# Kernel optimization log

Measured on AMD Instinct MI355X. Metric: run time of the kernel, lower is better.

The kernel has to match this reference:

```python
import jax, jax.numpy as jnp
import numpy as np

D_MODEL = 1024
HEADS = 16


def setup_inputs() -> dict:
    key = jax.random.key(0)
    ks = jax.random.split(key, 5)
    S = 4096
    x = jax.random.normal(ks[0], (S, D_MODEL), dtype=jnp.float32)
    scale = 1.0 / np.sqrt(D_MODEL)
    Wq = jax.random.normal(ks[1], (D_MODEL, D_MODEL), dtype=jnp.float32) * scale
    Wk = jax.random.normal(ks[2], (D_MODEL, D_MODEL), dtype=jnp.float32) * scale
    Wv = jax.random.normal(ks[3], (D_MODEL, D_MODEL), dtype=jnp.float32) * scale
    Wo = jax.random.normal(ks[4], (D_MODEL, D_MODEL), dtype=jnp.float32) * scale
    return {"x": x, "Wq": Wq, "Wk": Wk, "Wv": Wv, "Wo": Wo}


def reference(x, Wq, Wk, Wv, Wo):
    # x: [S, D]; weights follow torch Linear convention y = x @ W.T
    S, D = x.shape
    H = HEADS
    d_k = D // H
    q = (x @ Wq.T).reshape(S, H, d_k)  # [S,H,dk]
    k = (x @ Wk.T).reshape(S, H, d_k)
    v = (x @ Wv.T).reshape(S, H, d_k)
    # logits: [H, S, S] = q k^T / sqrt(d_k)
    logits = jnp.einsum('shd,thd->hst', q, k) / jnp.sqrt(jnp.asarray(d_k, x.dtype))
    probs = jax.nn.softmax(logits, axis=-1)
    out = jnp.einsum('hst,thd->shd', probs, v).reshape(S, D)
    return out @ Wo.T
```

## Files before the change

### kernel.cpp

```cpp
#include <hip/hip_runtime.h>
#include <hip/hip_bf16.h>


typedef __bf16 bf16_t;
typedef __bf16 bf16x8 __attribute__((ext_vector_type(8)));
typedef __bf16 bf16x4 __attribute__((ext_vector_type(4)));
typedef float f32x4 __attribute__((ext_vector_type(4)));

#define D_MODEL 1024
#define SEQ 4096
#define HEADS 16
#define DK 64
#define QSCALE 0.1803368801111204f

__global__ void cast_kernel(const float* __restrict__ in, bf16_t* __restrict__ out, int n) {
    int i = (blockIdx.x * blockDim.x + threadIdx.x) * 4;
    if (i < n) {
        float4 v = *(const float4*)(in + i);
        bf16x4 o;
        o[0] = (bf16_t)v.x; o[1] = (bf16_t)v.y; o[2] = (bf16_t)v.z; o[3] = (bf16_t)v.w;
        *(bf16x4*)(out + i) = o;
    }
}

__global__ void cast4_kernel(const float* __restrict__ a, const float* __restrict__ b,
                             const float* __restrict__ c, const float* __restrict__ d,
                             bf16_t* __restrict__ out) {
    int gi = blockIdx.x * blockDim.x + threadIdx.x;
    int which = gi >> 18;
    int i = (gi & 0x3FFFF) * 4;
    const float* src = which == 0 ? a : which == 1 ? b : which == 2 ? c : d;
    float4 v = *(const float4*)(src + i);
    bf16x4 o;
    o[0] = (bf16_t)v.x; o[1] = (bf16_t)v.y; o[2] = (bf16_t)v.z; o[3] = (bf16_t)v.w;
    *(bf16x4*)(out + (size_t)which * D_MODEL * D_MODEL + i) = o;
}

__device__ __forceinline__ void g2l16(const bf16_t* g, bf16_t* l) {
    __builtin_amdgcn_global_load_lds(
        (const __attribute__((address_space(1))) void*)g,
        (__attribute__((address_space(3))) void*)l, 16, 0, 0);
}

__device__ __forceinline__ bf16x8 exp2_pk(const f32x4 a, const f32x4 b) {
    int v[8];
#pragma unroll
    for (int r = 0; r < 4; r++) {
        v[r]     = (int)fmaf(a[r], 128.0f, 16250.99f);
        v[r + 4] = (int)fmaf(b[r], 128.0f, 16250.99f);
    }
    union { int u[4]; bf16x8 h; } o;
#pragma unroll
    for (int p = 0; p < 4; p++) o.u[p] = v[2 * p] | (v[2 * p + 1] << 16);
    return o.h;
}

template <int ROUTE>
__global__ __launch_bounds__(256, 4) void gemm_lds(const bf16_t* __restrict__ A,
                                                   const bf16_t* __restrict__ B,
                                                   void* __restrict__ out0,
                                                   void* __restrict__ out1,
                                                   void* __restrict__ out2,
                                                   int M, int N, int K) {
    __shared__ __align__(16) bf16_t As[128 * 64];
    __shared__ __align__(16) bf16_t Bs[64 * 64];

    const int tid = threadIdx.x;
    const int lane = tid & 63;
    const int wave = tid >> 6;
    const int l15 = lane & 15;
    const int lg  = lane >> 4;
    const int m0 = blockIdx.y * 128;
    const int n0 = blockIdx.x * 64;
    const int wm = (wave >> 1) * 64;
    const int wn = (wave & 1) * 32;

    const bf16_t* aSrc[4]; bf16_t* aDst[4];
#pragma unroll
    for (int it = 0; it < 4; it++) {
        int c = it * 256 + tid;
        int row = c >> 3, cc = (c & 7) ^ (row & 7);
        aSrc[it] = A + (size_t)(m0 + row) * K + cc * 8;
        aDst[it] = As + c * 8;
    }
    const bf16_t* bSrc[2]; bf16_t* bDst[2];
#pragma unroll
    for (int it = 0; it < 2; it++) {
        int c = it * 256 + tid;
        int row = c >> 3, cc = (c & 7) ^ (row & 7);
        bSrc[it] = B + (size_t)(n0 + row) * K + cc * 8;
        bDst[it] = Bs + c * 8;
    }

    int aoff[2][4], boff[2][2];
#pragma unroll
    for (int kk = 0; kk < 2; kk++) {
#pragma unroll
        for (int i = 0; i < 4; i++) {
            int row = wm + i * 16 + l15;
            aoff[kk][i] = row * 64 + (((kk << 2) | lg) ^ (row & 7)) * 8;
        }
#pragma unroll
        for (int j = 0; j < 2; j++) {
            int row = wn + j * 16 + l15;
            boff[kk][j] = row * 64 + (((kk << 2) | lg) ^ (row & 7)) * 8;
        }
    }

    f32x4 acc[4][2];
#pragma unroll
    for (int i = 0; i < 4; i++)
#pragma unroll
        for (int j = 0; j < 2; j++) acc[i][j] = f32x4{0.f, 0.f, 0.f, 0.f};

    for (int k0 = 0; k0 < K; k0 += 64) {
#pragma unroll
        for (int it = 0; it < 4; it++) g2l16(aSrc[it] + k0, aDst[it]);
#pragma unroll
        for (int it = 0; it < 2; it++) g2l16(bSrc[it] + k0, bDst[it]);
        __syncthreads();

#pragma unroll
        for (int kk = 0; kk < 2; kk++) {
            bf16x8 af[4], bfm[2];
#pragma unroll
            for (int i = 0; i < 4; i++) af[i] = *(const bf16x8*)(As + aoff[kk][i]);
#pragma unroll
            for (int j = 0; j < 2; j++) bfm[j] = *(const bf16x8*)(Bs + boff[kk][j]);
#pragma unroll
            for (int i = 0; i < 4; i++)
#pragma unroll
                for (int j = 0; j < 2; j++)
                    acc[i][j] = __builtin_amdgcn_mfma_f32_16x16x32_bf16(af[i], bfm[j], acc[i][j], 0, 0, 0);
        }
        __syncthreads();
    }

    const int ng = n0 + wn;
    if (ROUTE == 0) {
        float* C = (float*)out0;
#pragma unroll
        for (int i = 0; i < 4; i++)
#pragma unroll
            for (int r = 0; r < 4; r++) {
                int m = m0 + wm + i * 16 + lg * 4 + r;
                float* crow = C + (size_t)m * N + ng;
#pragma unroll
                for (int j = 0; j < 2; j++) crow[j * 16 + l15] = acc[i][j][r];
            }
    } else {
        if (ng < 2048) {
            const bool isQ = (ng < 1024);
            const float sc = isQ ? QSCALE : 1.0f;
            bf16_t* dst = isQ ? (bf16_t*)out0 : (bf16_t*)out1;
            int nn = ng & 1023;
#pragma unroll
            for (int i = 0; i < 4; i++)
#pragma unroll
                for (int r = 0; r < 4; r++) {
                    int m = m0 + wm + i * 16 + lg * 4 + r;
                    bf16_t* crow = dst + (size_t)m * D_MODEL + nn;
#pragma unroll
                    for (int j = 0; j < 2; j++) crow[j * 16 + l15] = (bf16_t)(acc[i][j][r] * sc);
                }
        } else {
            bf16_t* Vt = (bf16_t*)out2;
#pragma unroll
            for (int i = 0; i < 4; i++)
#pragma unroll
                for (int j = 0; j < 2; j++) {
                    int vcol = ng - 2048 + j * 16 + l15;
                    int m = m0 + wm + i * 16 + lg * 4;
                    int mp = (m & ~31) | (((m >> 2) & 3) << 3) | (((m >> 4) & 1) << 2);
                    bf16x4 v4;
#pragma unroll
                    for (int r = 0; r < 4; r++) v4[r] = (bf16_t)acc[i][j][r];
                    *(bf16x4*)(Vt + (size_t)vcol * SEQ + mp) = v4;
                }
        }
    }
}

__global__ __launch_bounds__(256) void attn_kernel(const bf16_t* __restrict__ Q,
                                                   const bf16_t* __restrict__ Km,
                                                   const bf16_t* __restrict__ Vt,
                                                   bf16_t* __restrict__ O) {
    const int tid = threadIdx.x;
    const int lane = tid & 63;
    const int wave = tid >> 6;
    const int l15 = lane & 15;
    const int lg  = lane >> 4;
    const int bid = blockIdx.x;
    const int h    = (bid & 7) * 2 + ((bid >> 3) & 1);
    const int qblk = bid >> 4;
    const int q0 = qblk * 128;
    const int hoff = h * DK;

    __shared__ union {
        struct { __align__(16) bf16_t K[2][64 * 64]; __align__(16) bf16_t V[2][64 * 64]; } kv;
        __align__(16) bf16_t Ot[128][72];
    } sm;

    bf16x8 qf[2][2];
#pragma unroll
    for (int t = 0; t < 2; t++)
#pragma unroll
        for (int c = 0; c < 2; c++)
            qf[t][c] = *(const bf16x8*)(Q + (size_t)(q0 + wave * 32 + t * 16 + l15) * D_MODEL
                                        + hoff + c * 32 + lg * 8);

    f32x4 oacc[2][4], lfrag[2];
#pragma unroll
    for (int t = 0; t < 2; t++) {
        lfrag[t] = f32x4{0.f, 0.f, 0.f, 0.f};
#pragma unroll
        for (int dt = 0; dt < 4; dt++) oacc[t][dt] = f32x4{0.f, 0.f, 0.f, 0.f};
    }

    bf16x8 ones8;
#pragma unroll
    for (int j = 0; j < 8; j++) ones8[j] = (bf16_t)1.0f;

    const bf16_t* kSrc[2]; const bf16_t* vSrc[2];
#pragma unroll
    for (int it = 0; it < 2; it++) {
        int c = it * 256 + tid;
        int row = c >> 3, dc = (c & 7) ^ (row & 7);
        kSrc[it] = Km + (size_t)row * D_MODEL + hoff + dc * 8;
        vSrc[it] = Vt + (size_t)(hoff + row) * SEQ + dc * 8;
    }

    int kOff[4][2], vOff[2][4];
#pragma unroll
    for (int kt = 0; kt < 4; kt++)
#pragma unroll
        for (int c = 0; c < 2; c++) {
            int row = kt * 16 + l15;
            kOff[kt][c] = row * 64 + (((c * 4 + lg) ^ (row & 7)) * 8);
        }
#pragma unroll
    for (int kp = 0; kp < 2; kp++)
#pragma unroll
        for (int dt = 0; dt < 4; dt++) {
            int row = dt * 16 + l15;
            vOff[kp][dt] = row * 64 + (((kp * 4 + lg) ^ (row & 7)) * 8);
        }

#pragma unroll
    for (int it = 0; it < 2; it++) {
        g2l16(kSrc[it], &sm.kv.K[0][(it * 256 + tid) * 8]);
        g2l16(vSrc[it], &sm.kv.V[0][(it * 256 + tid) * 8]);
    }

    for (int s = 0; s < SEQ / 64; s++) {
        const int cur = s & 1;
        __syncthreads();

        if (s + 1 < SEQ / 64) {
            const int nxt = cur ^ 1;
#pragma unroll
            for (int it = 0; it < 2; it++) {
                g2l16(kSrc[it] + (size_t)(s + 1) * 64 * D_MODEL, &sm.kv.K[nxt][(it * 256 + tid) * 8]);
                g2l16(vSrc[it] + (s + 1) * 64,                   &sm.kv.V[nxt][(it * 256 + tid) * 8]);
            }
        }

        const bf16_t* Kb = sm.kv.K[cur];
        const bf16_t* Vb = sm.kv.V[cur];

#pragma unroll
        for (int kp = 0; kp < 2; kp++) {
            f32x4 st[2][2];
#pragma unroll
            for (int sub = 0; sub < 2; sub++) {
                const int kt = kp * 2 + sub;
                const bf16x8 kf0 = *(const bf16x8*)(Kb + kOff[kt][0]);
                const bf16x8 kf1 = *(const bf16x8*)(Kb + kOff[kt][1]);
#pragma unroll
                for (int t = 0; t < 2; t++) {
                    f32x4 a = f32x4{0.f, 0.f, 0.f, 0.f};
                    a = __builtin_amdgcn_mfma_f32_16x16x32_bf16(kf0, qf[t][0], a, 0, 0, 0);
                    a = __builtin_amdgcn_mfma_f32_16x16x32_bf16(kf1, qf[t][1], a, 0, 0, 0);
                    st[t][sub] = a;
                }
            }

            const bf16x8 pbig0 = exp2_pk(st[0][0], st[0][1]);
            const bf16x8 pbig1 = exp2_pk(st[1][0], st[1][1]);

            lfrag[0] = __builtin_amdgcn_mfma_f32_16x16x32_bf16(ones8, pbig0, lfrag[0], 0, 0, 0);
            lfrag[1] = __builtin_amdgcn_mfma_f32_16x16x32_bf16(ones8, pbig1, lfrag[1], 0, 0, 0);

#pragma unroll
            for (int dt = 0; dt < 4; dt++) {
                const bf16x8 vf = *(const bf16x8*)(Vb + vOff[kp][dt]);
                oacc[0][dt] = __builtin_amdgcn_mfma_f32_16x16x32_bf16(vf, pbig0, oacc[0][dt], 0, 0, 0);
                oacc[1][dt] = __builtin_amdgcn_mfma_f32_16x16x32_bf16(vf, pbig1, oacc[1][dt], 0, 0, 0);
            }
        }
    }
    __syncthreads();

#pragma unroll
    for (int t = 0; t < 2; t++) {
        float inv = 1.f / lfrag[t][0];
        const int qrow = wave * 32 + t * 16 + l15;
#pragma unroll
        for (int dt = 0; dt < 4; dt++)
#pragma unroll
            for (int r = 0; r < 4; r++)
                sm.Ot[qrow][dt * 16 + lg * 4 + r] = (bf16_t)(oacc[t][dt][r] * inv);
    }
    __syncthreads();

    {
        const int row = tid >> 1;
        const int half = tid & 1;
        bf16_t* orow = O + (size_t)(q0 + row) * D_MODEL + hoff + half * 32;
#pragma unroll
        for (int m = 0; m < 4; m++)
            *(bf16x8*)(orow + m * 8) = *(const bf16x8*)(&sm.Ot[row][half * 32 + m * 8]);
    }
}

extern "C" void kernel_launch(void* const* d_in, const int* in_sizes, int n_in,
                              void* d_out, int out_size, void* d_ws, size_t ws_size,
                              hipStream_t stream) {
    const float* x  = (const float*)d_in[0];
    const float* Wq = (const float*)d_in[1];
    const float* Wk = (const float*)d_in[2];
    const float* Wv = (const float*)d_in[3];
    const float* Wo = (const float*)d_in[4];
    float* out = (float*)d_out;

    char* ws = (char*)d_ws;
    bf16_t* xb  = (bf16_t*)(ws);
    bf16_t* wqb = (bf16_t*)(ws + (8u  << 20));
    bf16_t* wob = (bf16_t*)(ws + (14u << 20));
    bf16_t* Qb  = (bf16_t*)(ws + (16u << 20));
    bf16_t* Kb  = (bf16_t*)(ws + (24u << 20));
    bf16_t* Vtb = (bf16_t*)(ws + (32u << 20));
    bf16_t* Ab  = (bf16_t*)(ws + (40u << 20));

    const int nX = SEQ * D_MODEL;
    cast_kernel<<<nX / 4 / 256, 256, 0, stream>>>(x, xb, nX);
    cast4_kernel<<<4 * 1024, 256, 0, stream>>>(Wq, Wk, Wv, Wo, wqb);

    gemm_lds<1><<<dim3(3 * D_MODEL / 64, SEQ / 128), 256, 0, stream>>>(
        xb, wqb, Qb, Kb, Vtb, SEQ, 3 * D_MODEL, D_MODEL);

    attn_kernel<<<512, 256, 0, stream>>>(Qb, Kb, Vtb, Ab);

    gemm_lds<0><<<dim3(D_MODEL / 64, SEQ / 128), 256, 0, stream>>>(
        Ab, wob, out, nullptr, nullptr, SEQ, D_MODEL, D_MODEL);
}
```

Baseline: 213.0 us.

## Load attention K/V fragments directly from global into registers, drop LDS staging

The attention kernel no longer stages K and V tiles through LDS with barriers. Each wave now loads its MFMA fragments straight from global memory into registers, double-buffered across two register sets. The output epilogue also writes directly instead of transposing through shared memory, and the exp2 approximation is rewritten to use a float magic-add plus a byte-permute pack. This removes LDS traffic and __syncthreads, but every wave in a block now re-reads the same K/V from global/L2, and register pressure rises, which is why occupancy is lowered to 2.

```diff
diff --git a/kernel.cpp b/kernel.cpp
--- a/kernel.cpp
+++ b/kernel.cpp
@@ -12,6 +12,7 @@
 #define HEADS 16
 #define DK 64
 #define QSCALE 0.1803368801111204f
+#define EXP2_MAGIC 8404859.0f
 
 __global__ void cast_kernel(const float* __restrict__ in, bf16_t* __restrict__ out, int n) {
     int i = (blockIdx.x * blockDim.x + threadIdx.x) * 4;
@@ -43,15 +44,16 @@
 }
 
 __device__ __forceinline__ bf16x8 exp2_pk(const f32x4 a, const f32x4 b) {
-    int v[8];
+    union { float f; unsigned u; } v[8];
 #pragma unroll
     for (int r = 0; r < 4; r++) {
-        v[r]     = (int)fmaf(a[r], 128.0f, 16250.99f);
-        v[r + 4] = (int)fmaf(b[r], 128.0f, 16250.99f);
-    }
-    union { int u[4]; bf16x8 h; } o;
-#pragma unroll
-    for (int p = 0; p < 4; p++) o.u[p] = v[2 * p] | (v[2 * p + 1] << 16);
+        v[r].f     = fmaf(a[r], 128.0f, EXP2_MAGIC);
+        v[r + 4].f = fmaf(b[r], 128.0f, EXP2_MAGIC);
+    }
+    union { unsigned u[4]; bf16x8 h; } o;
+#pragma unroll
+    for (int p = 0; p < 4; p++)
+        o.u[p] = __builtin_amdgcn_perm(v[2 * p + 1].u, v[2 * p].u, 0x05040100u);
     return o.h;
 }
 
@@ -181,10 +183,59 @@
     }
 }
 
-__global__ __launch_bounds__(256) void attn_kernel(const bf16_t* __restrict__ Q,
-                                                   const bf16_t* __restrict__ Km,
-                                                   const bf16_t* __restrict__ Vt,
-                                                   bf16_t* __restrict__ O) {
+struct Frags {
+    bf16x8 kf[4][2];
+    bf16x8 vf[2][4];
+};
+
+__device__ __forceinline__ void load_frags(Frags& f, const bf16_t* __restrict__ kB,
+                                           const bf16_t* __restrict__ vB, int s) {
+    const bf16_t* kS = kB + (size_t)s * 64 * D_MODEL;
+    const bf16_t* vS = vB + (size_t)s * 64;
+#pragma unroll
+    for (int kt = 0; kt < 4; kt++)
+#pragma unroll
+        for (int c = 0; c < 2; c++)
+            f.kf[kt][c] = *(const bf16x8*)(kS + (size_t)kt * 16 * D_MODEL + c * 32);
+#pragma unroll
+    for (int kp = 0; kp < 2; kp++)
+#pragma unroll
+        for (int dt = 0; dt < 4; dt++)
+            f.vf[kp][dt] = *(const bf16x8*)(vS + (size_t)dt * 16 * SEQ + kp * 32);
+}
+
+__device__ __forceinline__ void compute_step(const Frags& f, const bf16x8 (&qf)[2][2],
+                                             f32x4 (&oacc)[2][4], f32x4 (&lfrag)[2],
+                                             const bf16x8 ones8) {
+#pragma unroll
+    for (int kp = 0; kp < 2; kp++) {
+        f32x4 st[2][2];
+#pragma unroll
+        for (int sub = 0; sub < 2; sub++) {
+            const int kt = kp * 2 + sub;
+#pragma unroll
+            for (int t = 0; t < 2; t++) {
+                f32x4 a = f32x4{0.f, 0.f, 0.f, 0.f};
+                a = __builtin_amdgcn_mfma_f32_16x16x32_bf16(f.kf[kt][0], qf[t][0], a, 0, 0, 0);
+                a = __builtin_amdgcn_mfma_f32_16x16x32_bf16(f.kf[kt][1], qf[t][1], a, 0, 0, 0);
+                st[t][sub] = a;
+            }
+        }
+#pragma unroll
+        for (int t = 0; t < 2; t++) {
+            const bf16x8 pbig = exp2_pk(st[t][0], st[t][1]);
+            lfrag[t] = __builtin_amdgcn_mfma_f32_16x16x32_bf16(ones8, pbig, lfrag[t], 0, 0, 0);
+#pragma unroll
+            for (int dt = 0; dt < 4; dt++)
+                oacc[t][dt] = __builtin_amdgcn_mfma_f32_16x16x32_bf16(f.vf[kp][dt], pbig, oacc[t][dt], 0, 0, 0);
+        }
+    }
+}
+
+__global__ __launch_bounds__(256, 2) void attn_kernel(const bf16_t* __restrict__ Q,
+                                                      const bf16_t* __restrict__ Km,
+                                                      const bf16_t* __restrict__ Vt,
+                                                      bf16_t* __restrict__ O) {
     const int tid = threadIdx.x;
     const int lane = tid & 63;
     const int wave = tid >> 6;
@@ -196,11 +247,6 @@
     const int q0 = qblk * 128;
     const int hoff = h * DK;
 
-    __shared__ union {
-        struct { __align__(16) bf16_t K[2][64 * 64]; __align__(16) bf16_t V[2][64 * 64]; } kv;
-        __align__(16) bf16_t Ot[128][72];
-    } sm;
-
     bf16x8 qf[2][2];
 #pragma unroll
     for (int t = 0; t < 2; t++)
@@ -221,105 +267,30 @@
 #pragma unroll
     for (int j = 0; j < 8; j++) ones8[j] = (bf16_t)1.0f;
 
-    const bf16_t* kSrc[2]; const bf16_t* vSrc[2];
-#pragma unroll
-    for (int it = 0; it < 2; it++) {
-        int c = it * 256 + tid;
-        int row = c >> 3, dc = (c & 7) ^ (row & 7);
-        kSrc[it] = Km + (size_t)row * D_MODEL + hoff + dc * 8;
-        vSrc[it] = Vt + (size_t)(hoff + row) * SEQ + dc * 8;
-    }
-
-    int kOff[4][2], vOff[2][4];
-#pragma unroll
-    for (int kt = 0; kt < 4; kt++)
-#pragma unroll
-        for (int c = 0; c < 2; c++) {
-            int row = kt * 16 + l15;
-            kOff[kt][c] = row * 64 + (((c * 4 + lg) ^ (row & 7)) * 8);
-        }
-#pragma unroll
-    for (int kp = 0; kp < 2; kp++)
+    const bf16_t* kB = Km + (size_t)l15 * D_MODEL + hoff + lg * 8;
+    const bf16_t* vB = Vt + (size_t)(hoff + l15) * SEQ + lg * 8;
+
+    Frags fA, fB;
+    load_frags(fA, kB, vB, 0);
+
+    for (int s = 0; s < SEQ / 64; s += 2) {
+        load_frags(fB, kB, vB, s + 1);
+        compute_step(fA, qf, oacc, lfrag, ones8);
+        if (s + 2 < SEQ / 64) load_frags(fA, kB, vB, s + 2);
+        compute_step(fB, qf, oacc, lfrag, ones8);
+    }
+
+#pragma unroll
+    for (int t = 0; t < 2; t++) {
+        const float inv = 1.f / lfrag[t][0];
+        const size_t qrow = (size_t)(q0 + wave * 32 + t * 16 + l15);
 #pragma unroll
         for (int dt = 0; dt < 4; dt++) {
-            int row = dt * 16 + l15;
-            vOff[kp][dt] = row * 64 + (((kp * 4 + lg) ^ (row & 7)) * 8);
-        }
-
-#pragma unroll
-    for (int it = 0; it < 2; it++) {
-        g2l16(kSrc[it], &sm.kv.K[0][(it * 256 + tid) * 8]);
-        g2l16(vSrc[it], &sm.kv.V[0][(it * 256 + tid) * 8]);
-    }
-
-    for (int s = 0; s < SEQ / 64; s++) {
-        const int cur = s & 1;
-        __syncthreads();
-
-        if (s + 1 < SEQ / 64) {
-            const int nxt = cur ^ 1;
-#pragma unroll
-            for (int it = 0; it < 2; it++) {
-                g2l16(kSrc[it] + (size_t)(s + 1) * 64 * D_MODEL, &sm.kv.K[nxt][(it * 256 + tid) * 8]);
-                g2l16(vSrc[it] + (s + 1) * 64,                   &sm.kv.V[nxt][(it * 256 + tid) * 8]);
-            }
-        }
-
-        const bf16_t* Kb = sm.kv.K[cur];
-        const bf16_t* Vb = sm.kv.V[cur];
-
-#pragma unroll
-        for (int kp = 0; kp < 2; kp++) {
-            f32x4 st[2][2];
-#pragma unroll
-            for (int sub = 0; sub < 2; sub++) {
-                const int kt = kp * 2 + sub;
-                const bf16x8 kf0 = *(const bf16x8*)(Kb + kOff[kt][0]);
-                const bf16x8 kf1 = *(const bf16x8*)(Kb + kOff[kt][1]);
-#pragma unroll
-                for (int t = 0; t < 2; t++) {
-                    f32x4 a = f32x4{0.f, 0.f, 0.f, 0.f};
-                    a = __builtin_amdgcn_mfma_f32_16x16x32_bf16(kf0, qf[t][0], a, 0, 0, 0);
-                    a = __builtin_amdgcn_mfma_f32_16x16x32_bf16(kf1, qf[t][1], a, 0, 0, 0);
-                    st[t][sub] = a;
-                }
-            }
-
-            const bf16x8 pbig0 = exp2_pk(st[0][0], st[0][1]);
-            const bf16x8 pbig1 = exp2_pk(st[1][0], st[1][1]);
-
-            lfrag[0] = __builtin_amdgcn_mfma_f32_16x16x32_bf16(ones8, pbig0, lfrag[0], 0, 0, 0);
-            lfrag[1] = __builtin_amdgcn_mfma_f32_16x16x32_bf16(ones8, pbig1, lfrag[1], 0, 0, 0);
-
-#pragma unroll
-            for (int dt = 0; dt < 4; dt++) {
-                const bf16x8 vf = *(const bf16x8*)(Vb + vOff[kp][dt]);
-                oacc[0][dt] = __builtin_amdgcn_mfma_f32_16x16x32_bf16(vf, pbig0, oacc[0][dt], 0, 0, 0);
-                oacc[1][dt] = __builtin_amdgcn_mfma_f32_16x16x32_bf16(vf, pbig1, oacc[1][dt], 0, 0, 0);
-            }
-        }
-    }
-    __syncthreads();
-
-#pragma unroll
-    for (int t = 0; t < 2; t++) {
-        float inv = 1.f / lfrag[t][0];
-        const int qrow = wave * 32 + t * 16 + l15;
-#pragma unroll
-        for (int dt = 0; dt < 4; dt++)
-#pragma unroll
-            for (int r = 0; r < 4; r++)
-                sm.Ot[qrow][dt * 16 + lg * 4 + r] = (bf16_t)(oacc[t][dt][r] * inv);
-    }
-    __syncthreads();
-
-    {
-        const int row = tid >> 1;
-        const int half = tid & 1;
-        bf16_t* orow = O + (size_t)(q0 + row) * D_MODEL + hoff + half * 32;
-#pragma unroll
-        for (int m = 0; m < 4; m++)
-            *(bf16x8*)(orow + m * 8) = *(const bf16x8*)(&sm.Ot[row][half * 32 + m * 8]);
+            bf16x4 o4;
+#pragma unroll
+            for (int r = 0; r < 4; r++) o4[r] = (bf16_t)(oacc[t][dt][r] * inv);
+            *(bf16x4*)(O + qrow * D_MODEL + hoff + dt * 16 + lg * 4) = o4;
+        }
     }
 }
 
```

After: 356.3 us. 1.67x slower.

## Double per-block query tile in attention and streamline exp2 packing

Applied to the files above, without the earlier changes.

The attention kernel now handles 256 query rows per block (64 per wave) instead of 128, so each K/V tile loaded into LDS is reused across twice as many queries, and the grid shrinks to 256 blocks. The exp2 approximation switches from float-to-int conversion to a magic-constant add plus a byte-permute packing, which needs fewer instructions. The output is written straight from registers rather than staged through LDS. In exchange, register pressure rises and there are half as many blocks, so fewer waves are available to hide latency, with only one block per CU in the launch bounds.

```diff
diff --git a/kernel.cpp b/kernel.cpp
--- a/kernel.cpp
+++ b/kernel.cpp
@@ -12,6 +12,7 @@
 #define HEADS 16
 #define DK 64
 #define QSCALE 0.1803368801111204f
+#define EXP2_MAGIC 8404859.0f
 
 __global__ void cast_kernel(const float* __restrict__ in, bf16_t* __restrict__ out, int n) {
     int i = (blockIdx.x * blockDim.x + threadIdx.x) * 4;
@@ -43,15 +44,16 @@
 }
 
 __device__ __forceinline__ bf16x8 exp2_pk(const f32x4 a, const f32x4 b) {
-    int v[8];
+    union { float f; unsigned u; } v[8];
 #pragma unroll
     for (int r = 0; r < 4; r++) {
-        v[r]     = (int)fmaf(a[r], 128.0f, 16250.99f);
-        v[r + 4] = (int)fmaf(b[r], 128.0f, 16250.99f);
-    }
-    union { int u[4]; bf16x8 h; } o;
-#pragma unroll
-    for (int p = 0; p < 4; p++) o.u[p] = v[2 * p] | (v[2 * p + 1] << 16);
+        v[r].f     = fmaf(a[r], 128.0f, EXP2_MAGIC);
+        v[r + 4].f = fmaf(b[r], 128.0f, EXP2_MAGIC);
+    }
+    union { unsigned u[4]; bf16x8 h; } o;
+#pragma unroll
+    for (int p = 0; p < 4; p++)
+        o.u[p] = __builtin_amdgcn_perm(v[2 * p + 1].u, v[2 * p].u, 0x05040100u);
     return o.h;
 }
 
@@ -181,10 +183,10 @@
     }
 }
 
-__global__ __launch_bounds__(256) void attn_kernel(const bf16_t* __restrict__ Q,
-                                                   const bf16_t* __restrict__ Km,
-                                                   const bf16_t* __restrict__ Vt,
-                                                   bf16_t* __restrict__ O) {
+__global__ __launch_bounds__(256, 1) void attn_kernel(const bf16_t* __restrict__ Q,
+                                                      const bf16_t* __restrict__ Km,
+                                                      const bf16_t* __restrict__ Vt,
+                                                      bf16_t* __restrict__ O) {
     const int tid = threadIdx.x;
     const int lane = tid & 63;
     const int wave = tid >> 6;
@@ -193,25 +195,25 @@
     const int bid = blockIdx.x;
     const int h    = (bid & 7) * 2 + ((bid >> 3) & 1);
     const int qblk = bid >> 4;
-    const int q0 = qblk * 128;
+    const int q0 = qblk * 256;
     const int hoff = h * DK;
 
-    __shared__ union {
-        struct { __align__(16) bf16_t K[2][64 * 64]; __align__(16) bf16_t V[2][64 * 64]; } kv;
-        __align__(16) bf16_t Ot[128][72];
+    __shared__ struct {
+        __align__(16) bf16_t K[2][64 * 64];
+        __align__(16) bf16_t V[2][64 * 64];
     } sm;
 
-    bf16x8 qf[2][2];
-#pragma unroll
-    for (int t = 0; t < 2; t++)
+    bf16x8 qf[4][2];
+#pragma unroll
+    for (int t = 0; t < 4; t++)
 #pragma unroll
         for (int c = 0; c < 2; c++)
-            qf[t][c] = *(const bf16x8*)(Q + (size_t)(q0 + wave * 32 + t * 16 + l15) * D_MODEL
+            qf[t][c] = *(const bf16x8*)(Q + (size_t)(q0 + wave * 64 + t * 16 + l15) * D_MODEL
                                         + hoff + c * 32 + lg * 8);
 
-    f32x4 oacc[2][4], lfrag[2];
-#pragma unroll
-    for (int t = 0; t < 2; t++) {
+    f32x4 oacc[4][4], lfrag[4];
+#pragma unroll
+    for (int t = 0; t < 4; t++) {
         lfrag[t] = f32x4{0.f, 0.f, 0.f, 0.f};
 #pragma unroll
         for (int dt = 0; dt < 4; dt++) oacc[t][dt] = f32x4{0.f, 0.f, 0.f, 0.f};
@@ -248,8 +250,8 @@
 
 #pragma unroll
     for (int it = 0; it < 2; it++) {
-        g2l16(kSrc[it], &sm.kv.K[0][(it * 256 + tid) * 8]);
-        g2l16(vSrc[it], &sm.kv.V[0][(it * 256 + tid) * 8]);
+        g2l16(kSrc[it], &sm.K[0][(it * 256 + tid) * 8]);
+        g2l16(vSrc[it], &sm.V[0][(it * 256 + tid) * 8]);
     }
 
     for (int s = 0; s < SEQ / 64; s++) {
@@ -260,24 +262,28 @@
             const int nxt = cur ^ 1;
 #pragma unroll
             for (int it = 0; it < 2; it++) {
-                g2l16(kSrc[it] + (size_t)(s + 1) * 64 * D_MODEL, &sm.kv.K[nxt][(it * 256 + tid) * 8]);
-                g2l16(vSrc[it] + (s + 1) * 64,                   &sm.kv.V[nxt][(it * 256 + tid) * 8]);
+                g2l16(kSrc[it] + (size_t)(s + 1) * 64 * D_MODEL, &sm.K[nxt][(it * 256 + tid) * 8]);
+                g2l16(vSrc[it] + (s + 1) * 64,                   &sm.V[nxt][(it * 256 + tid) * 8]);
             }
         }
 
-        const bf16_t* Kb = sm.kv.K[cur];
-        const bf16_t* Vb = sm.kv.V[cur];
+        const bf16_t* Kb = sm.K[cur];
+        const bf16_t* Vb = sm.V[cur];
 
 #pragma unroll
         for (int kp = 0; kp < 2; kp++) {
-            f32x4 st[2][2];
+            bf16x8 vf[4];
+#pragma unroll
+            for (int dt = 0; dt < 4; dt++) vf[dt] = *(const bf16x8*)(Vb + vOff[kp][dt]);
+
+            f32x4 st[4][2];
 #pragma unroll
             for (int sub = 0; sub < 2; sub++) {
                 const int kt = kp * 2 + sub;
                 const bf16x8 kf0 = *(const bf16x8*)(Kb + kOff[kt][0]);
                 const bf16x8 kf1 = *(const bf16x8*)(Kb + kOff[kt][1]);
 #pragma unroll
-                for (int t = 0; t < 2; t++) {
+                for (int t = 0; t < 4; t++) {
                     f32x4 a = f32x4{0.f, 0.f, 0.f, 0.f};
                     a = __builtin_amdgcn_mfma_f32_16x16x32_bf16(kf0, qf[t][0], a, 0, 0, 0);
                     a = __builtin_amdgcn_mfma_f32_16x16x32_bf16(kf1, qf[t][1], a, 0, 0, 0);
@@ -285,41 +291,28 @@
                 }
             }
 
-            const bf16x8 pbig0 = exp2_pk(st[0][0], st[0][1]);
-            const bf16x8 pbig1 = exp2_pk(st[1][0], st[1][1]);
-
-            lfrag[0] = __builtin_amdgcn_mfma_f32_16x16x32_bf16(ones8, pbig0, lfrag[0], 0, 0, 0);
-            lfrag[1] = __builtin_amdgcn_mfma_f32_16x16x32_bf16(ones8, pbig1, lfrag[1], 0, 0, 0);
-
-#pragma unroll
-            for (int dt = 0; dt < 4; dt++) {
-                const bf16x8 vf = *(const bf16x8*)(Vb + vOff[kp][dt]);
-                oacc[0][dt] = __builtin_amdgcn_mfma_f32_16x16x32_bf16(vf, pbig0, oacc[0][dt], 0, 0, 0);
-                oacc[1][dt] = __builtin_amdgcn_mfma_f32_16x16x32_bf16(vf, pbig1, oacc[1][dt], 0, 0, 0);
+#pragma unroll
+            for (int t = 0; t < 4; t++) {
+                const bf16x8 pbig = exp2_pk(st[t][0], st[t][1]);
+                lfrag[t] = __builtin_amdgcn_mfma_f32_16x16x32_bf16(ones8, pbig, lfrag[t], 0, 0, 0);
+#pragma unroll
+                for (int dt = 0; dt < 4; dt++)
+                    oacc[t][dt] = __builtin_amdgcn_mfma_f32_16x16x32_bf16(vf[dt], pbig, oacc[t][dt], 0, 0, 0);
             }
         }
     }
-    __syncthreads();
-
-#pragma unroll
-    for (int t = 0; t < 2; t++) {
-        float inv = 1.f / lfrag[t][0];
-        const int qrow = wave * 32 + t * 16 + l15;
-#pragma unroll
-        for (int dt = 0; dt < 4; dt++)
-#pragma unroll
-            for (int r = 0; r < 4; r++)
-                sm.Ot[qrow][dt * 16 + lg * 4 + r] = (bf16_t)(oacc[t][dt][r] * inv);
-    }
-    __syncthreads();
-
-    {
-        const int row = tid >> 1;
-        const int half = tid & 1;
-        bf16_t* orow = O + (size_t)(q0 + row) * D_MODEL + hoff + half * 32;
-#pragma unroll
-        for (int m = 0; m < 4; m++)
-            *(bf16x8*)(orow + m * 8) = *(const bf16x8*)(&sm.Ot[row][half * 32 + m * 8]);
+
+#pragma unroll
+    for (int t = 0; t < 4; t++) {
+        const float inv = 1.f / lfrag[t][0];
+        const size_t qrow = (size_t)(q0 + wave * 64 + t * 16 + l15);
+#pragma unroll
+        for (int dt = 0; dt < 4; dt++) {
+            bf16x4 o4;
+#pragma unroll
+            for (int r = 0; r < 4; r++) o4[r] = (bf16_t)(oacc[t][dt][r] * inv);
+            *(bf16x4*)(O + qrow * D_MODEL + hoff + dt * 16 + lg * 4) = o4;
+        }
     }
 }
 
@@ -349,7 +342,7 @@
     gemm_lds<1><<<dim3(3 * D_MODEL / 64, SEQ / 128), 256, 0, stream>>>(
         xb, wqb, Qb, Kb, Vtb, SEQ, 3 * D_MODEL, D_MODEL);
 
-    attn_kernel<<<512, 256, 0, stream>>>(Qb, Kb, Vtb, Ab);
+    attn_kernel<<<256, 256, 0, stream>>>(Qb, Kb, Vtb, Ab);
 
     gemm_lds<0><<<dim3(D_MODEL / 64, SEQ / 128), 256, 0, stream>>>(
         Ab, wob, out, nullptr, nullptr, SEQ, D_MODEL, D_MODEL);
```

Measured after the change: 200.1 us. 6.1% less time.
